# Kernel optimization log

Hardware: AMD Instinct MI355X
Metric: run time of the kernel (lower is better)

## Reference

```python
import jax, jax.numpy as jnp
import numpy as np
from jax import lax


def _rnn_layer(x_tbd, h0, Wh, bh, Wo, bo):
    """Run one RNNBlock over time. x_tbd: [T,B,D], h0: [B,H]. Returns [T,B,out]."""
    def step(h, xt):
        c = jnp.concatenate([xt, h], axis=1)        # [B, D+H]
        h_new = jnp.tanh(c @ Wh + bh)               # [B, H]
        o = jnp.tanh(c @ Wo + bo)                   # [B, out]
        return h_new, o
    _, out = lax.scan(step, h0, x_tbd)
    return out


def setup_inputs() -> dict:
    key = jax.random.key(0)
    ks = jax.random.split(key, 10)
    B, T, D, H = 64, 256, 512, 512
    s = 0.03  # small init so tanh stays non-saturated
    return {
        "x": jax.random.normal(ks[0], (B, T, D), dtype=jnp.float32),
        "encoder_output": jax.random.normal(ks[1], (B, H), dtype=jnp.float32),
        "Wh0": jax.random.normal(ks[2], (D + H, H), dtype=jnp.float32) * s,
        "bh0": jax.random.normal(ks[3], (H,), dtype=jnp.float32) * s,
        "Wo0": jax.random.normal(ks[4], (D + H, D), dtype=jnp.float32) * s,
        "bo0": jax.random.normal(ks[5], (D,), dtype=jnp.float32) * s,
        "Wh1": jax.random.normal(ks[6], (D + H, H), dtype=jnp.float32) * s,
        "bh1": jax.random.normal(ks[7], (H,), dtype=jnp.float32) * s,
        "Wo1": jax.random.normal(ks[8], (D + H, D), dtype=jnp.float32) * s,
        "bo1": jax.random.normal(ks[9], (D,), dtype=jnp.float32) * s,
    }


def reference(x, encoder_output, Wh0, bh0, Wo0, bo0, Wh1, bh1, Wo1, bo1):
    B = x.shape[0]
    H1 = Wh1.shape[1]
    x_tbd = jnp.transpose(x, (1, 0, 2))                       # [T,B,D]
    # Layer 0: initial hidden = encoder_output
    out0 = _rnn_layer(x_tbd, encoder_output, Wh0, bh0, Wo0, bo0)
    # Layer 1: hidden reset to zeros (hidden=None in torch source)
    h0 = jnp.zeros((B, H1), dtype=x.dtype)
    out1 = _rnn_layer(out0, h0, Wh1, bh1, Wo1, bo1)
    return jnp.transpose(out1, (1, 0, 2))                     # [B,T,D]
```

## Files before the change

### kernel.cpp

```cpp
#include <hip/hip_runtime.h>
#include <hip/hip_bf16.h>
#include <hip/hip_fp16.h>

typedef unsigned int u32;
typedef unsigned short u16;
typedef short s16x8 __attribute__((ext_vector_type(8)));
typedef float f32x4 __attribute__((ext_vector_type(4)));
typedef _Float16 f16x2 __attribute__((ext_vector_type(2)));

#define T_STEPS 256

__device__ __forceinline__ u16 f2bu(float f) {
  return __bfloat16_as_ushort(__float2bfloat16(f));
}
__device__ __forceinline__ float fast_tanh(float x) {
  float ax = fabsf(x);
  float e = __expf(-2.f * ax);
  float r = 1.f - 2.f * e / (1.f + e);
  return copysignf(r, x);
}
__device__ __forceinline__ __half2 bch2(u32 v) {
  return __builtin_bit_cast(__half2, v);
}
__device__ __forceinline__ void gload_lds16(const void* g, void* l) {
  __builtin_amdgcn_global_load_lds((const __attribute__((address_space(1))) u32*)g,
                                   (__attribute__((address_space(3))) u32*)l, 16, 0, 0);
}

__global__ void k_cvt_bf16(const float* __restrict__ in, u16* __restrict__ out, int n4) {
  int i = blockIdx.x * blockDim.x + threadIdx.x;
  if (i >= n4) return;
  const float4 v = ((const float4*)in)[i];
  ushort4 o;
  o.x = f2bu(v.x); o.y = f2bu(v.y); o.z = f2bu(v.z); o.w = f2bu(v.w);
  ((ushort4*)out)[i] = o;
}

__global__ void k_prep_w(const float* __restrict__ Wh, const float* __restrict__ Wo,
                         u16* __restrict__ BcatT, u16* __restrict__ WhoT,
                         u32* __restrict__ Wpack) {
  int idx = blockIdx.x * 256 + threadIdx.x;
  if (idx < 1024 * 512) {
    int n = idx >> 9, k = idx & 511;
    float v = (n < 512) ? Wh[k * 512 + n] : Wo[k * 512 + (n - 512)];
    BcatT[idx] = f2bu(v);
  } else if (idx < 1024 * 512 + 512 * 512) {
    int t = idx - 1024 * 512;
    int n = t >> 9, k = t & 511;
    WhoT[t] = f2bu(Wo[(512 + k) * 512 + n]);
  } else {
    int t = idx - (1024 * 512 + 512 * 512);
    int k2 = t >> 9, j = t & 511;
    u16 a = __half_as_ushort(__float2half(Wh[(512 + 2 * k2) * 512 + j]));
    u16 b = __half_as_ushort(__float2half(Wh[(512 + 2 * k2 + 1) * 512 + j]));
    Wpack[t] = (u32)a | ((u32)b << 16);
  }
}

template <int MODE>
__global__ __launch_bounds__(256) void k_gemm(
    const u16* __restrict__ A, const u16* __restrict__ BT, int NX,
    __half* __restrict__ outH, u16* __restrict__ outB, float* __restrict__ outF,
    const __half* __restrict__ Uo, const float* __restrict__ biasH,
    const float* __restrict__ biasO) {
  __shared__ __align__(16) u16 As[128 * 64], Bs[128 * 64];
  const int bid = blockIdx.x;
  const int bn = bid % NX, bm = bid / NX;
  const int m0 = bm * 128, n0 = bn * 128;
  const int tid = threadIdx.x, w = tid >> 6, l = tid & 63;
  const int l15 = l & 15, lk = (l >> 4) << 3;
  f32x4 acc[4][4] = {};
  for (int kt = 0; kt < 8; ++kt) {
    const int k0 = kt * 64;
#pragma unroll
    for (int i = 0; i < 4; ++i) {
      int idx = w * 4 + i;
      int ob = idx * 1024 + l * 16;
      int row = ob >> 7, cb = ob & 127;
      int scb = cb ^ ((row & 7) << 4);
      gload_lds16((const char*)A + (size_t)(m0 + row) * 1024 + k0 * 2 + scb,
                  (char*)As + idx * 1024);
      gload_lds16((const char*)BT + (size_t)(n0 + row) * 1024 + k0 * 2 + scb,
                  (char*)Bs + idx * 1024);
    }
    __syncthreads();
    const int wr = (w >> 1) * 64, wc = (w & 1) * 64;
#pragma unroll
    for (int kk = 0; kk < 2; ++kk) {
      s16x8 af[4], bfr[4];
      const int kb = (kk * 32 + lk) * 2;
#pragma unroll
      for (int i = 0; i < 4; ++i) {
        int ar = wr + i * 16 + l15;
        af[i] = *(const s16x8*)((const char*)As + ar * 128 + (kb ^ ((ar & 7) << 4)));
        int br = wc + i * 16 + l15;
        bfr[i] = *(const s16x8*)((const char*)Bs + br * 128 + (kb ^ ((br & 7) << 4)));
      }
#pragma unroll
      for (int i = 0; i < 4; ++i)
#pragma unroll
        for (int jj = 0; jj < 4; ++jj)
          acc[i][jj] = __builtin_amdgcn_mfma_f32_16x16x32_bf16(af[i], bfr[jj], acc[i][jj], 0, 0, 0);
    }
    __syncthreads();
  }
#pragma unroll
  for (int i = 0; i < 4; ++i)
#pragma unroll
    for (int jj = 0; jj < 4; ++jj)
#pragma unroll
      for (int rr = 0; rr < 4; ++rr) {
        int row = m0 + (w >> 1) * 64 + i * 16 + ((l >> 4) << 2) + rr;
        int col = n0 + (w & 1) * 64 + jj * 16 + l15;
        float v = acc[i][jj][rr];
        if (MODE == 0) {
          float bsv = (col < 512) ? biasH[col] : biasO[col - 512];
          outH[(size_t)row * 1024 + col] = __float2half(v + bsv);
        } else {
          float o = fast_tanh(v + __half2float(Uo[(size_t)row * 1024 + col]));
          if (MODE == 1) outB[(size_t)row * 512 + col] = f2bu(o);
          else           outF[(size_t)row * 512 + col] = o;
        }
      }
}

#define REG_P 192
#define LDS_GRP 16
#define SCAN_LDS_BYTES (LDS_GRP * 8192 + 2048)

__global__ __launch_bounds__(512, 2)
void k_scan(const u32* __restrict__ Wpack, const __half* __restrict__ Uh,
            const float* __restrict__ h0, u16* __restrict__ Hseq) {
  extern __shared__ __align__(16) u32 smem[];
  u32* Wl = smem;
  __half* hb = (__half*)(smem + LDS_GRP * 2048);
  const int b = blockIdx.x, j = threadIdx.x;
  u32 wreg[REG_P];
#pragma unroll
  for (int p = 0; p < REG_P; ++p) wreg[p] = Wpack[p * 512 + j];
#pragma unroll
  for (int g = 0; g < LDS_GRP; ++g)
#pragma unroll
    for (int q = 0; q < 4; ++q)
      Wl[g * 2048 + j * 4 + q] = Wpack[(REG_P + 4 * g + q) * 512 + j];
  float h = h0 ? h0[b * 512 + j] : 0.f;
  hb[j] = __float2half(h);
  __syncthreads();
  const int r0 = b * T_STEPS;
  float u_cur = __half2float(Uh[(size_t)r0 * 1024 + j]);
  for (int t = 0; t < T_STEPS; ++t) {
    const int r = r0 + t;
    const int rn = (t < T_STEPS - 1) ? r + 1 : r;
    float u_nxt = __half2float(Uh[(size_t)rn * 1024 + j]);
    Hseq[(size_t)r * 512 + j] = f2bu(h);
    const uint4* h4 = (const uint4*)(hb + (t & 1) * 512);
    __half2 a0 = __float2half2_rn(0.f), a1 = a0, a2 = a0, a3 = a0;
#pragma unroll
    for (int g = 0; g < 48; ++g) {
      uint4 hv = h4[g];
      a0 = __hfma2(bch2(wreg[4 * g + 0]), bch2(hv.x), a0);
      a1 = __hfma2(bch2(wreg[4 * g + 1]), bch2(hv.y), a1);
      a2 = __hfma2(bch2(wreg[4 * g + 2]), bch2(hv.z), a2);
      a3 = __hfma2(bch2(wreg[4 * g + 3]), bch2(hv.w), a3);
    }
#pragma unroll
    for (int g = 0; g < LDS_GRP; ++g) {
      uint4 hv = h4[48 + g];
      uint4 wv = *(const uint4*)&Wl[g * 2048 + j * 4];
      a0 = __hfma2(bch2(wv.x), bch2(hv.x), a0);
      a1 = __hfma2(bch2(wv.y), bch2(hv.y), a1);
      a2 = __hfma2(bch2(wv.z), bch2(hv.z), a2);
      a3 = __hfma2(bch2(wv.w), bch2(hv.w), a3);
    }
    float acc = u_cur;
    acc += __low2float(a0) + __high2float(a0);
    acc += __low2float(a1) + __high2float(a1);
    acc += __low2float(a2) + __high2float(a2);
    acc += __low2float(a3) + __high2float(a3);
    float hn = fast_tanh(acc);
    hb[((t + 1) & 1) * 512 + j] = __float2half(hn);
    h = hn;
    u_cur = u_nxt;
    __syncthreads();
  }
}

extern "C" void kernel_launch(void* const* d_in, const int* in_sizes, int n_in,
                              void* d_out, int out_size, void* d_ws, size_t ws_size,
                              hipStream_t stream) {
  const float* x   = (const float*)d_in[0];
  const float* enc = (const float*)d_in[1];
  const float* Wh0 = (const float*)d_in[2];
  const float* bh0 = (const float*)d_in[3];
  const float* Wo0 = (const float*)d_in[4];
  const float* bo0 = (const float*)d_in[5];
  const float* Wh1 = (const float*)d_in[6];
  const float* bh1 = (const float*)d_in[7];
  const float* Wo1 = (const float*)d_in[8];
  const float* bo1 = (const float*)d_in[9];
  char* ws = (char*)d_ws;
  u16*    Xbf   = (u16*)(ws);
  __half* U     = (__half*)(ws + 16777216);
  u16*    Hs0   = (u16*)(ws + 16777216 + 33554432);
  u16*    Out0  = (u16*)(ws + 16777216 + 33554432 + 16777216);
  u16*    Hs1   = (u16*)(ws + 16777216 + 33554432 + 2 * 16777216);
  char*   wb    = ws + 16777216 + 33554432 + 3 * 16777216;
  u16*    Bct0  = (u16*)(wb);
  u16*    WhoT0 = (u16*)(wb + 1048576);
  u32*    Wpk0  = (u32*)(wb + 1048576 + 524288);
  u16*    Bct1  = (u16*)(wb + 1048576 + 2 * 524288);
  u16*    WhoT1 = (u16*)(wb + 2 * 1048576 + 2 * 524288);
  u32*    Wpk1  = (u32*)(wb + 2 * 1048576 + 3 * 524288);

  (void)hipFuncSetAttribute((const void*)k_scan,
                            hipFuncAttributeMaxDynamicSharedMemorySize,
                            SCAN_LDS_BYTES);

  k_cvt_bf16<<<8192, 256, 0, stream>>>(x, Xbf, 8388608 / 4);
  k_prep_w<<<3584, 256, 0, stream>>>(Wh0, Wo0, Bct0, WhoT0, Wpk0);
  k_prep_w<<<3584, 256, 0, stream>>>(Wh1, Wo1, Bct1, WhoT1, Wpk1);
  k_gemm<0><<<1024, 256, 0, stream>>>(Xbf, Bct0, 8, U, nullptr, nullptr, nullptr, bh0, bo0);
  k_scan<<<64, 512, SCAN_LDS_BYTES, stream>>>(Wpk0, U, enc, Hs0);
  k_gemm<1><<<512, 256, 0, stream>>>(Hs0, WhoT0, 4, nullptr, Out0, nullptr, U + 512, nullptr, nullptr);
  k_gemm<0><<<1024, 256, 0, stream>>>(Out0, Bct1, 8, U, nullptr, nullptr, nullptr, bh1, bo1);
  k_scan<<<64, 512, SCAN_LDS_BYTES, stream>>>(Wpk1, U, nullptr, Hs1);
  k_gemm<2><<<512, 256, 0, stream>>>(Hs1, WhoT1, 4, nullptr, nullptr, (float*)d_out, U + 512, nullptr, nullptr);
}
```

Baseline: 1.027 ms.

## Fuse both RNN scans and intermediate GEMMs into one pipelined cooperative kernel

After: 1.109 ms. 8.0% more time.

```diff
diff --git a/kernel.cpp b/kernel.cpp
--- a/kernel.cpp
+++ b/kernel.cpp
@@ -25,6 +25,13 @@
 __device__ __forceinline__ void gload_lds16(const void* g, void* l) {
   __builtin_amdgcn_global_load_lds((const __attribute__((address_space(1))) u32*)g,
                                    (__attribute__((address_space(3))) u32*)l, 16, 0, 0);
+}
+__device__ __forceinline__ void wg_wait_ge(const u32* p, u32 target) {
+  if (threadIdx.x == 0) {
+    while (__hip_atomic_load(p, __ATOMIC_ACQUIRE, __HIP_MEMORY_SCOPE_AGENT) < target)
+      __builtin_amdgcn_s_sleep(16);
+  }
+  __syncthreads();
 }
 
 __global__ void k_cvt_bf16(const float* __restrict__ in, u16* __restrict__ out, int n4) {
@@ -128,13 +135,13 @@
 #define LDS_GRP 16
 #define SCAN_LDS_BYTES (LDS_GRP * 8192 + 2048)
 
-__global__ __launch_bounds__(512, 2)
-void k_scan(const u32* __restrict__ Wpack, const __half* __restrict__ Uh,
-            const float* __restrict__ h0, u16* __restrict__ Hseq) {
-  extern __shared__ __align__(16) u32 smem[];
+__device__ void scan_role(u32* smem, const u32* __restrict__ Wpack,
+                          const __half* __restrict__ Uh, const float* __restrict__ h0,
+                          u16* __restrict__ Hseq, int b,
+                          u32* rel, const u32* pollv) {
   u32* Wl = smem;
   __half* hb = (__half*)(smem + LDS_GRP * 2048);
-  const int b = blockIdx.x, j = threadIdx.x;
+  const int j = threadIdx.x;
   u32 wreg[REG_P];
 #pragma unroll
   for (int p = 0; p < REG_P; ++p) wreg[p] = Wpack[p * 512 + j];
@@ -146,13 +153,18 @@
   float h = h0 ? h0[b * 512 + j] : 0.f;
   hb[j] = __float2half(h);
   __syncthreads();
-  const int r0 = b * T_STEPS;
-  float u_cur = __half2float(Uh[(size_t)r0 * 1024 + j]);
+  const size_t r0 = (size_t)b * T_STEPS;
+  float u_cur = 0.f;
   for (int t = 0; t < T_STEPS; ++t) {
-    const int r = r0 + t;
-    const int rn = (t < T_STEPS - 1) ? r + 1 : r;
-    float u_nxt = __half2float(Uh[(size_t)rn * 1024 + j]);
-    Hseq[(size_t)r * 512 + j] = f2bu(h);
+    const size_t r = r0 + t;
+    if ((t & 31) == 0) {
+      if (pollv) wg_wait_ge(pollv + (size_t)(t >> 5) * 16, 8u);
+      if (rel && t && j == 0)
+        __hip_atomic_store(rel, (u32)t, __ATOMIC_RELEASE, __HIP_MEMORY_SCOPE_AGENT);
+      u_cur = __half2float(Uh[r * 1024 + j]);
+    }
+    Hseq[r * 512 + j] = f2bu(h);
+    float u_nxt = ((t & 31) != 31) ? __half2float(Uh[(r + 1) * 1024 + j]) : 0.f;
     const uint4* h4 = (const uint4*)(hb + (t & 1) * 512);
     __half2 a0 = __float2half2_rn(0.f), a1 = a0, a2 = a0, a3 = a0;
 #pragma unroll
@@ -182,6 +194,98 @@
     h = hn;
     u_cur = u_nxt;
     __syncthreads();
+  }
+  if (rel && j == 0)
+    __hip_atomic_store(rel, 256u, __ATOMIC_RELEASE, __HIP_MEMORY_SCOPE_AGENT);
+}
+
+__device__ void helper_role(int hid, __half* __restrict__ U,
+                            const u16* __restrict__ Hs0, u16* __restrict__ Out0,
+                            const u16* __restrict__ WhoT0, const u16* __restrict__ Bct1,
+                            const float* __restrict__ bh1, const float* __restrict__ bo1,
+                            u32* prog0, u32* o0done, u32* u1done) {
+  const int tid = threadIdx.x;
+  const int w = tid >> 6, l = tid & 63;
+  const int wr = w >> 2, wc = w & 3, l15 = l & 15, lk8 = (l >> 4) * 8;
+  for (int id = hid; id < 6144; id += 128) {
+    const int tb = id / 768, loc = id % 768;
+    if (loc < 256) {
+      const int b = loc >> 2, cq = loc & 3;
+      wg_wait_ge(prog0 + (size_t)b * 16, (u32)(32 * (tb + 1)));
+      const int r0 = b * 256 + tb * 32, c0 = cq * 128;
+      const int arow = r0 + wr * 16 + l15;
+      const int bc0 = c0 + wc * 32 + l15, bc1 = bc0 + 16;
+      f32x4 a0 = {}, a1 = {};
+#pragma unroll
+      for (int k0 = 0; k0 < 512; k0 += 32) {
+        s16x8 av = *(const s16x8*)&Hs0[(size_t)arow * 512 + k0 + lk8];
+        s16x8 b0 = *(const s16x8*)&WhoT0[(size_t)bc0 * 512 + k0 + lk8];
+        s16x8 b1 = *(const s16x8*)&WhoT0[(size_t)bc1 * 512 + k0 + lk8];
+        a0 = __builtin_amdgcn_mfma_f32_16x16x32_bf16(av, b0, a0, 0, 0, 0);
+        a1 = __builtin_amdgcn_mfma_f32_16x16x32_bf16(av, b1, a1, 0, 0, 0);
+      }
+#pragma unroll
+      for (int rr = 0; rr < 4; ++rr) {
+        int row = r0 + wr * 16 + (l >> 4) * 4 + rr;
+        int cA = c0 + wc * 32 + l15, cB = cA + 16;
+        float vA = fast_tanh(a0[rr] + __half2float(U[(size_t)row * 1024 + 512 + cA]));
+        float vB = fast_tanh(a1[rr] + __half2float(U[(size_t)row * 1024 + 512 + cB]));
+        Out0[(size_t)row * 512 + cA] = f2bu(vA);
+        Out0[(size_t)row * 512 + cB] = f2bu(vB);
+      }
+      __syncthreads();
+      if (tid == 0)
+        __hip_atomic_fetch_add(o0done + ((size_t)b * 8 + tb) * 16, 1u,
+                               __ATOMIC_RELEASE, __HIP_MEMORY_SCOPE_AGENT);
+    } else {
+      const int loc2 = loc - 256;
+      const int b = loc2 >> 3, cc = loc2 & 7;
+      wg_wait_ge(o0done + ((size_t)b * 8 + tb) * 16, 4u);
+      const int r0 = b * 256 + tb * 32, c0 = cc * 128;
+      const int arow = r0 + wr * 16 + l15;
+      const int bc0 = c0 + wc * 32 + l15, bc1 = bc0 + 16;
+      f32x4 a0 = {}, a1 = {};
+#pragma unroll
+      for (int k0 = 0; k0 < 512; k0 += 32) {
+        s16x8 av = *(const s16x8*)&Out0[(size_t)arow * 512 + k0 + lk8];
+        s16x8 b0 = *(const s16x8*)&Bct1[(size_t)bc0 * 512 + k0 + lk8];
+        s16x8 b1 = *(const s16x8*)&Bct1[(size_t)bc1 * 512 + k0 + lk8];
+        a0 = __builtin_amdgcn_mfma_f32_16x16x32_bf16(av, b0, a0, 0, 0, 0);
+        a1 = __builtin_amdgcn_mfma_f32_16x16x32_bf16(av, b1, a1, 0, 0, 0);
+      }
+#pragma unroll
+      for (int rr = 0; rr < 4; ++rr) {
+        int row = r0 + wr * 16 + (l >> 4) * 4 + rr;
+        int cA = c0 + wc * 32 + l15, cB = cA + 16;
+        float bA = (cA < 512) ? bh1[cA] : bo1[cA - 512];
+        float bB = (cB < 512) ? bh1[cB] : bo1[cB - 512];
+        U[(size_t)row * 1024 + cA] = __float2half(a0[rr] + bA);
+        U[(size_t)row * 1024 + cB] = __float2half(a1[rr] + bB);
+      }
+      __syncthreads();
+      if (tid == 0)
+        __hip_atomic_fetch_add(u1done + ((size_t)b * 8 + tb) * 16, 1u,
+                               __ATOMIC_RELEASE, __HIP_MEMORY_SCOPE_AGENT);
+    }
+  }
+}
+
+__global__ __launch_bounds__(512, 2) void k_mega(
+    const u32* __restrict__ Wpk0, const u32* __restrict__ Wpk1,
+    __half* __restrict__ U, const float* __restrict__ enc,
+    u16* __restrict__ Hs0, u16* __restrict__ Hs1, u16* __restrict__ Out0,
+    const u16* __restrict__ WhoT0, const u16* __restrict__ Bct1,
+    const float* __restrict__ bh1, const float* __restrict__ bo1,
+    u32* prog0, u32* o0done, u32* u1done) {
+  extern __shared__ __align__(16) u32 smem[];
+  const int wg = blockIdx.x;
+  if (wg < 64) {
+    scan_role(smem, Wpk0, U, enc, Hs0, wg, prog0 + (size_t)wg * 16, nullptr);
+  } else if (wg < 128) {
+    const int b = wg - 64;
+    scan_role(smem, Wpk1, U, nullptr, Hs1, b, nullptr, u1done + (size_t)b * 8 * 16);
+  } else {
+    helper_role(wg - 128, U, Hs0, Out0, WhoT0, Bct1, bh1, bo1, prog0, o0done, u1done);
   }
 }
 
@@ -199,30 +303,43 @@
   const float* Wo1 = (const float*)d_in[8];
   const float* bo1 = (const float*)d_in[9];
   char* ws = (char*)d_ws;
-  u16*    Xbf   = (u16*)(ws);
-  __half* U     = (__half*)(ws + 16777216);
-  u16*    Hs0   = (u16*)(ws + 16777216 + 33554432);
-  u16*    Out0  = (u16*)(ws + 16777216 + 33554432 + 16777216);
-  u16*    Hs1   = (u16*)(ws + 16777216 + 33554432 + 2 * 16777216);
-  char*   wb    = ws + 16777216 + 33554432 + 3 * 16777216;
+  __half* U    = (__half*)(ws);
+  u16*    Hs0  = (u16*)(ws + 33554432);
+  u16*    Hs1  = (u16*)(ws + 33554432 + 16777216);
+  u16*    XO   = (u16*)(ws + 33554432 + 2 * 16777216);
+  char*   wb   = ws + 33554432 + 3 * 16777216;
   u16*    Bct0  = (u16*)(wb);
   u16*    WhoT0 = (u16*)(wb + 1048576);
   u32*    Wpk0  = (u32*)(wb + 1048576 + 524288);
   u16*    Bct1  = (u16*)(wb + 1048576 + 2 * 524288);
   u16*    WhoT1 = (u16*)(wb + 2 * 1048576 + 2 * 524288);
   u32*    Wpk1  = (u32*)(wb + 2 * 1048576 + 3 * 524288);
-
-  (void)hipFuncSetAttribute((const void*)k_scan,
+  u32*    cnt   = (u32*)(wb + 2 * 1048576 + 4 * 524288);
+  u32*    prog0  = cnt;
+  u32*    o0done = cnt + 1024;
+  u32*    u1done = cnt + 1024 + 8192;
+
+  (void)hipFuncSetAttribute((const void*)k_mega,
                             hipFuncAttributeMaxDynamicSharedMemorySize,
                             SCAN_LDS_BYTES);
 
-  k_cvt_bf16<<<8192, 256, 0, stream>>>(x, Xbf, 8388608 / 4);
+  hipMemsetAsync(cnt, 0, (1024 + 2 * 8192) * 4, stream);
+  k_cvt_bf16<<<8192, 256, 0, stream>>>(x, XO, 8388608 / 4);
   k_prep_w<<<3584, 256, 0, stream>>>(Wh0, Wo0, Bct0, WhoT0, Wpk0);
   k_prep_w<<<3584, 256, 0, stream>>>(Wh1, Wo1, Bct1, WhoT1, Wpk1);
-  k_gemm<0><<<1024, 256, 0, stream>>>(Xbf, Bct0, 8, U, nullptr, nullptr, nullptr, bh0, bo0);
-  k_scan<<<64, 512, SCAN_LDS_BYTES, stream>>>(Wpk0, U, enc, Hs0);
-  k_gemm<1><<<512, 256, 0, stream>>>(Hs0, WhoT0, 4, nullptr, Out0, nullptr, U + 512, nullptr, nullptr);
-  k_gemm<0><<<1024, 256, 0, stream>>>(Out0, Bct1, 8, U, nullptr, nullptr, nullptr, bh1, bo1);
-  k_scan<<<64, 512, SCAN_LDS_BYTES, stream>>>(Wpk1, U, nullptr, Hs1);
-  k_gemm<2><<<512, 256, 0, stream>>>(Hs1, WhoT1, 4, nullptr, nullptr, (float*)d_out, U + 512, nullptr, nullptr);
-}
+  k_gemm<0><<<1024, 256, 0, stream>>>(XO, Bct0, 8, U, nullptr, nullptr, nullptr, bh0, bo0);
+
+  {
+    const u32* a0 = Wpk0; const u32* a1 = Wpk1; __half* a2 = U;
+    const float* a3 = enc; u16* a4 = Hs0; u16* a5 = Hs1; u16* a6 = XO;
+    const u16* a7 = WhoT0; const u16* a8 = Bct1;
+    const float* a9 = bh1; const float* a10 = bo1;
+    u32* a11 = prog0; u32* a12 = o0done; u32* a13 = u1done;
+    void* args[] = {&a0, &a1, &a2, &a3, &a4, &a5, &a6, &a7, &a8, &a9, &a10, &a11, &a12, &a13};
+    hipLaunchCooperativeKernel((const void*)k_mega, dim3(256), dim3(512), args,
+                               SCAN_LDS_BYTES, stream);
+  }
+
+  k_gemm<2><<<512, 256, 0, stream>>>(Hs1, WhoT1, 4, nullptr, nullptr, (float*)d_out,
+                                     U + 512, nullptr, nullptr);
+}
```

## Split recurrent scan K-dimension across 8 lanes with DPP reduction and streamed weights

Applied to the files above, without the earlier changes.

Result: slower. 1.620 ms (+57.8%).

```diff
diff --git a/kernel.cpp b/kernel.cpp
--- a/kernel.cpp
+++ b/kernel.cpp
@@ -6,7 +6,6 @@
 typedef unsigned short u16;
 typedef short s16x8 __attribute__((ext_vector_type(8)));
 typedef float f32x4 __attribute__((ext_vector_type(4)));
-typedef _Float16 f16x2 __attribute__((ext_vector_type(2)));
 
 #define T_STEPS 256
 
@@ -25,6 +24,11 @@
 __device__ __forceinline__ void gload_lds16(const void* g, void* l) {
   __builtin_amdgcn_global_load_lds((const __attribute__((address_space(1))) u32*)g,
                                    (__attribute__((address_space(3))) u32*)l, 16, 0, 0);
+}
+template <int CTRL>
+__device__ __forceinline__ float dppadd(float x) {
+  int r = __builtin_amdgcn_update_dpp(0, __builtin_bit_cast(int, x), CTRL, 0xf, 0xf, true);
+  return x + __builtin_bit_cast(float, r);
 }
 
 __global__ void k_cvt_bf16(const float* __restrict__ in, u16* __restrict__ out, int n4) {
@@ -49,11 +53,25 @@
     int n = t >> 9, k = t & 511;
     WhoT[t] = f2bu(Wo[(512 + k) * 512 + n]);
   } else {
-    int t = idx - (1024 * 512 + 512 * 512);
-    int k2 = t >> 9, j = t & 511;
-    u16 a = __half_as_ushort(__float2half(Wh[(512 + 2 * k2) * 512 + j]));
-    u16 b = __half_as_ushort(__float2half(Wh[(512 + 2 * k2 + 1) * 512 + j]));
-    Wpack[t] = (u32)a | ((u32)b << 16);
+    int w2 = idx - (1024 * 512 + 512 * 512);
+    int p, i, j;
+    if (w2 < 65536) {
+      p = w2 >> 13; i = (w2 >> 9) & 15; j = w2 & 511;
+    } else if (w2 < 81920) {
+      int t = w2 - 65536;
+      p = t >> 11; j = (t >> 2) & 511; i = 16 + (t & 3);
+    } else {
+      int t = w2 - 81920;
+      int row = t >> 11;
+      p = row / 3; int g = row - 3 * p;
+      j = (t >> 2) & 511; i = 20 + g * 4 + (t & 3);
+    }
+    int ks = j & 7, c = j >> 3;
+    int C = p * 64 + c;
+    int k = ks * 64 + 2 * i;
+    u16 a = __half_as_ushort(__float2half(Wh[(512 + k) * 512 + C]));
+    u16 b = __half_as_ushort(__float2half(Wh[(512 + k + 1) * 512 + C]));
+    Wpack[w2] = (u32)a | ((u32)b << 16);
   }
 }
 
@@ -124,64 +142,108 @@
       }
 }
 
-#define REG_P 192
-#define LDS_GRP 16
-#define SCAN_LDS_BYTES (LDS_GRP * 8192 + 2048)
-
-__global__ __launch_bounds__(512, 2)
-void k_scan(const u32* __restrict__ Wpack, const __half* __restrict__ Uh,
-            const float* __restrict__ h0, u16* __restrict__ Hseq) {
+#define HB_SLICE 144
+#define HB_PAR (8 * HB_SLICE)
+#define SCAN3_LDS_BYTES (65536 + 2 * HB_PAR)
+
+__global__ __launch_bounds__(512) __attribute__((amdgpu_waves_per_eu(2, 2)))
+void k_scan3(const u32* __restrict__ Wpk, const __half* __restrict__ Uh,
+             const float* __restrict__ h0, u16* __restrict__ Hseq) {
   extern __shared__ __align__(16) u32 smem[];
   u32* Wl = smem;
-  __half* hb = (__half*)(smem + LDS_GRP * 2048);
+  char* hb = (char*)(smem + 16384);
   const int b = blockIdx.x, j = threadIdx.x;
-  u32 wreg[REG_P];
-#pragma unroll
-  for (int p = 0; p < REG_P; ++p) wreg[p] = Wpack[p * 512 + j];
-#pragma unroll
-  for (int g = 0; g < LDS_GRP; ++g)
-#pragma unroll
-    for (int q = 0; q < 4; ++q)
-      Wl[g * 2048 + j * 4 + q] = Wpack[(REG_P + 4 * g + q) * 512 + j];
-  float h = h0 ? h0[b * 512 + j] : 0.f;
-  hb[j] = __float2half(h);
+  const int ks = j & 7, c = j >> 3;
+  const size_t r0 = (size_t)b * T_STEPS;
+
+  u32 wreg[128];
+#pragma unroll
+  for (int p8 = 0; p8 < 128; ++p8) wreg[p8] = Wpk[p8 * 512 + j];
+  {
+    const u32* src = Wpk + 65536;
+#pragma unroll
+    for (int p = 0; p < 8; ++p)
+      gload_lds16(src + (p * 512 + j) * 4, (char*)Wl + (p * 512 + (j & ~63)) * 16);
+  }
+  {
+    float hv = h0 ? h0[b * 512 + j] : 0.f;
+    *(__half*)(hb + (j >> 6) * HB_SLICE + (j & 63) * 2) = __float2half(hv);
+    Hseq[r0 * 512 + j] = f2bu(hv);
+  }
+  const u32* Wst = Wpk + 81920;
+  u32 sbufA[12], sbufB[12];
+#pragma unroll
+  for (int g = 0; g < 3; ++g) {
+    uint4 v = *(const uint4*)(Wst + ((0 * 3 + g) * 512 + j) * 4);
+    sbufA[g * 4 + 0] = v.x; sbufA[g * 4 + 1] = v.y;
+    sbufA[g * 4 + 2] = v.z; sbufA[g * 4 + 3] = v.w;
+  }
+  float u_pre[8];
+#pragma unroll
+  for (int p = 0; p < 8; ++p) u_pre[p] = __half2float(Uh[r0 * 1024 + p * 64 + c]);
   __syncthreads();
-  const int r0 = b * T_STEPS;
-  float u_cur = __half2float(Uh[(size_t)r0 * 1024 + j]);
+
+  int par = 0;
   for (int t = 0; t < T_STEPS; ++t) {
-    const int r = r0 + t;
-    const int rn = (t < T_STEPS - 1) ? r + 1 : r;
-    float u_nxt = __half2float(Uh[(size_t)rn * 1024 + j]);
-    Hseq[(size_t)r * 512 + j] = f2bu(h);
-    const uint4* h4 = (const uint4*)(hb + (t & 1) * 512);
-    __half2 a0 = __float2half2_rn(0.f), a1 = a0, a2 = a0, a3 = a0;
-#pragma unroll
-    for (int g = 0; g < 48; ++g) {
-      uint4 hv = h4[g];
-      a0 = __hfma2(bch2(wreg[4 * g + 0]), bch2(hv.x), a0);
-      a1 = __hfma2(bch2(wreg[4 * g + 1]), bch2(hv.y), a1);
-      a2 = __hfma2(bch2(wreg[4 * g + 2]), bch2(hv.z), a2);
-      a3 = __hfma2(bch2(wreg[4 * g + 3]), bch2(hv.w), a3);
-    }
-#pragma unroll
-    for (int g = 0; g < LDS_GRP; ++g) {
-      uint4 hv = h4[48 + g];
-      uint4 wv = *(const uint4*)&Wl[g * 2048 + j * 4];
-      a0 = __hfma2(bch2(wv.x), bch2(hv.x), a0);
-      a1 = __hfma2(bch2(wv.y), bch2(hv.y), a1);
-      a2 = __hfma2(bch2(wv.z), bch2(hv.z), a2);
-      a3 = __hfma2(bch2(wv.w), bch2(hv.w), a3);
-    }
-    float acc = u_cur;
-    acc += __low2float(a0) + __high2float(a0);
-    acc += __low2float(a1) + __high2float(a1);
-    acc += __low2float(a2) + __high2float(a2);
-    acc += __low2float(a3) + __high2float(a3);
-    float hn = fast_tanh(acc);
-    hb[((t + 1) & 1) * 512 + j] = __float2half(hn);
-    h = hn;
-    u_cur = u_nxt;
+    u32 hsv[32];
+    {
+      const char* hbp = hb + par * HB_PAR + ks * HB_SLICE;
+#pragma unroll
+      for (int i = 0; i < 8; ++i) {
+        uint4 v = *(const uint4*)(hbp + i * 16);
+        hsv[i * 4 + 0] = v.x; hsv[i * 4 + 1] = v.y;
+        hsv[i * 4 + 2] = v.z; hsv[i * 4 + 3] = v.w;
+      }
+    }
+    float u_cur[8];
+#pragma unroll
+    for (int p = 0; p < 8; ++p) u_cur[p] = u_pre[p];
+    if (t + 1 < T_STEPS) {
+#pragma unroll
+      for (int p = 0; p < 8; ++p)
+        u_pre[p] = __half2float(Uh[(r0 + t + 1) * 1024 + p * 64 + c]);
+    }
+#pragma unroll
+    for (int p = 0; p < 8; ++p) {
+      u32* scur = (p & 1) ? sbufB : sbufA;
+      u32* snxt = (p & 1) ? sbufA : sbufB;
+#pragma unroll
+      for (int g = 0; g < 3; ++g) {
+        uint4 v = *(const uint4*)(Wst + ((((p + 1) & 7) * 3 + g) * 512 + j) * 4);
+        snxt[g * 4 + 0] = v.x; snxt[g * 4 + 1] = v.y;
+        snxt[g * 4 + 2] = v.z; snxt[g * 4 + 3] = v.w;
+      }
+      uint4 wlv = *(const uint4*)((const char*)Wl + (p * 512 + j) * 16);
+      u32 wlw[4] = {wlv.x, wlv.y, wlv.z, wlv.w};
+      __half2 a0 = __float2half2_rn(0.f), a1 = a0;
+#pragma unroll
+      for (int i = 0; i < 16; ++i) {
+        __half2& a = (i & 1) ? a1 : a0;
+        a = __hfma2(bch2(wreg[p * 16 + i]), bch2(hsv[i]), a);
+      }
+#pragma unroll
+      for (int i = 0; i < 4; ++i) {
+        __half2& a = (i & 1) ? a1 : a0;
+        a = __hfma2(bch2(wlw[i]), bch2(hsv[16 + i]), a);
+      }
+#pragma unroll
+      for (int i = 0; i < 12; ++i) {
+        __half2& a = (i & 1) ? a1 : a0;
+        a = __hfma2(bch2(scur[i]), bch2(hsv[20 + i]), a);
+      }
+      float sm = __low2float(a0) + __high2float(a0) +
+                 __low2float(a1) + __high2float(a1);
+      sm = dppadd<0xB1>(sm);
+      sm = dppadd<0x4E>(sm);
+      sm = dppadd<0x141>(sm);
+      float f = fast_tanh(sm + u_cur[p]);
+      if (ks == 0)
+        *(__half*)(hb + (par ^ 1) * HB_PAR + p * HB_SLICE + c * 2) = __float2half(f);
+      if (ks == 1 && t + 1 < T_STEPS)
+        Hseq[(r0 + t + 1) * 512 + p * 64 + c] = f2bu(f);
+    }
     __syncthreads();
+    par ^= 1;
   }
 }
 
@@ -212,17 +274,17 @@
   u16*    WhoT1 = (u16*)(wb + 2 * 1048576 + 2 * 524288);
   u32*    Wpk1  = (u32*)(wb + 2 * 1048576 + 3 * 524288);
 
-  (void)hipFuncSetAttribute((const void*)k_scan,
+  (void)hipFuncSetAttribute((const void*)k_scan3,
                             hipFuncAttributeMaxDynamicSharedMemorySize,
-                            SCAN_LDS_BYTES);
+                            SCAN3_LDS_BYTES);
 
   k_cvt_bf16<<<8192, 256, 0, stream>>>(x, Xbf, 8388608 / 4);
   k_prep_w<<<3584, 256, 0, stream>>>(Wh0, Wo0, Bct0, WhoT0, Wpk0);
   k_prep_w<<<3584, 256, 0, stream>>>(Wh1, Wo1, Bct1, WhoT1, Wpk1);
   k_gemm<0><<<1024, 256, 0, stream>>>(Xbf, Bct0, 8, U, nullptr, nullptr, nullptr, bh0, bo0);
-  k_scan<<<64, 512, SCAN_LDS_BYTES, stream>>>(Wpk0, U, enc, Hs0);
+  k_scan3<<<64, 512, SCAN3_LDS_BYTES, stream>>>(Wpk0, U, enc, Hs0);
   k_gemm<1><<<512, 256, 0, stream>>>(Hs0, WhoT0, 4, nullptr, Out0, nullptr, U + 512, nullptr, nullptr);
   k_gemm<0><<<1024, 256, 0, stream>>>(Out0, Bct1, 8, U, nullptr, nullptr, nullptr, bh1, bo1);
-  k_scan<<<64, 512, SCAN_LDS_BYTES, stream>>>(Wpk1, U, nullptr, Hs1);
+  k_scan3<<<64, 512, SCAN3_LDS_BYTES, stream>>>(Wpk1, U, nullptr, Hs1);
   k_gemm<2><<<512, 256, 0, stream>>>(Hs1, WhoT1, 4, nullptr, nullptr, (float*)d_out, U + 512, nullptr, nullptr);
 }
```

## Split recurrent dot product across 4 lanes with DPP reduction to cut LDS h reads

Applied to the files above, without the earlier changes.

After: 1.217 ms. +18.5%, slower.

```diff
diff --git a/kernel.cpp b/kernel.cpp
--- a/kernel.cpp
+++ b/kernel.cpp
@@ -6,7 +6,6 @@
 typedef unsigned short u16;
 typedef short s16x8 __attribute__((ext_vector_type(8)));
 typedef float f32x4 __attribute__((ext_vector_type(4)));
-typedef _Float16 f16x2 __attribute__((ext_vector_type(2)));
 
 #define T_STEPS 256
 
@@ -25,6 +24,11 @@
 __device__ __forceinline__ void gload_lds16(const void* g, void* l) {
   __builtin_amdgcn_global_load_lds((const __attribute__((address_space(1))) u32*)g,
                                    (__attribute__((address_space(3))) u32*)l, 16, 0, 0);
+}
+template <int CTRL>
+__device__ __forceinline__ float dppadd(float x) {
+  int r = __builtin_amdgcn_update_dpp(0, __builtin_bit_cast(int, x), CTRL, 0xf, 0xf, true);
+  return x + __builtin_bit_cast(float, r);
 }
 
 __global__ void k_cvt_bf16(const float* __restrict__ in, u16* __restrict__ out, int n4) {
@@ -49,11 +53,26 @@
     int n = t >> 9, k = t & 511;
     WhoT[t] = f2bu(Wo[(512 + k) * 512 + n]);
   } else {
-    int t = idx - (1024 * 512 + 512 * 512);
-    int k2 = t >> 9, j = t & 511;
-    u16 a = __half_as_ushort(__float2half(Wh[(512 + 2 * k2) * 512 + j]));
-    u16 b = __half_as_ushort(__float2half(Wh[(512 + 2 * k2 + 1) * 512 + j]));
-    Wpack[t] = (u32)a | ((u32)b << 16);
+    int w2 = idx - (1024 * 512 + 512 * 512);
+    int i, j, col;
+    if (w2 < 98304) {
+      int p = w2 >> 9; j = w2 & 511;
+      int g = p >> 4, r = p & 15;
+      col = r >> 2; int q = r & 3;
+      i = 4 * g + q;
+    } else {
+      int t = w2 - 98304;
+      int q = t & 3; j = (t >> 2) & 511;
+      int grp = t >> 11;
+      col = grp >> 2; int g2 = grp & 3;
+      i = 48 + g2 * 4 + q;
+    }
+    int ks = j & 3, c0 = j >> 2;
+    int C = col * 128 + c0;
+    int k = ks * 128 + 2 * i;
+    u16 a = __half_as_ushort(__float2half(Wh[(512 + k) * 512 + C]));
+    u16 b = __half_as_ushort(__float2half(Wh[(512 + k + 1) * 512 + C]));
+    Wpack[w2] = (u32)a | ((u32)b << 16);
   }
 }
 
@@ -124,64 +143,114 @@
       }
 }
 
-#define REG_P 192
-#define LDS_GRP 16
-#define SCAN_LDS_BYTES (LDS_GRP * 8192 + 2048)
+#define SCAN4_LDS_BYTES (131072 + 2048)
 
 __global__ __launch_bounds__(512, 2)
-void k_scan(const u32* __restrict__ Wpack, const __half* __restrict__ Uh,
-            const float* __restrict__ h0, u16* __restrict__ Hseq) {
+void k_scan4(const u32* __restrict__ Wpk, const __half* __restrict__ Uh,
+             const float* __restrict__ h0, u16* __restrict__ Hseq) {
   extern __shared__ __align__(16) u32 smem[];
-  u32* Wl = smem;
-  __half* hb = (__half*)(smem + LDS_GRP * 2048);
+  uint4* Wl4 = (uint4*)smem;
+  char* hb = (char*)smem + 131072;
   const int b = blockIdx.x, j = threadIdx.x;
-  u32 wreg[REG_P];
-#pragma unroll
-  for (int p = 0; p < REG_P; ++p) wreg[p] = Wpack[p * 512 + j];
-#pragma unroll
-  for (int g = 0; g < LDS_GRP; ++g)
-#pragma unroll
-    for (int q = 0; q < 4; ++q)
-      Wl[g * 2048 + j * 4 + q] = Wpack[(REG_P + 4 * g + q) * 512 + j];
-  float h = h0 ? h0[b * 512 + j] : 0.f;
-  hb[j] = __float2half(h);
+  const int ks = j & 3, c0 = j >> 2;
+  const size_t r0 = (size_t)b * T_STEPS;
+  u32 wreg[192];
+#pragma unroll
+  for (int p = 0; p < 192; ++p) wreg[p] = Wpk[p * 512 + j];
+#pragma unroll
+  for (int g = 0; g < 16; ++g)
+    Wl4[g * 512 + j] = *(const uint4*)(Wpk + 98304 + ((size_t)g * 512 + j) * 4);
+  {
+    float hv = h0 ? h0[b * 512 + j] : 0.f;
+    *(__half*)(hb + j * 2) = __float2half(hv);
+    Hseq[r0 * 512 + j] = f2bu(hv);
+  }
+  float u0 = __half2float(Uh[r0 * 1024 + c0]);
+  float u1 = __half2float(Uh[r0 * 1024 + 128 + c0]);
+  float u2 = __half2float(Uh[r0 * 1024 + 256 + c0]);
+  float u3 = __half2float(Uh[r0 * 1024 + 384 + c0]);
   __syncthreads();
-  const int r0 = b * T_STEPS;
-  float u_cur = __half2float(Uh[(size_t)r0 * 1024 + j]);
+  int par = 0;
   for (int t = 0; t < T_STEPS; ++t) {
-    const int r = r0 + t;
-    const int rn = (t < T_STEPS - 1) ? r + 1 : r;
-    float u_nxt = __half2float(Uh[(size_t)rn * 1024 + j]);
-    Hseq[(size_t)r * 512 + j] = f2bu(h);
-    const uint4* h4 = (const uint4*)(hb + (t & 1) * 512);
-    __half2 a0 = __float2half2_rn(0.f), a1 = a0, a2 = a0, a3 = a0;
-#pragma unroll
-    for (int g = 0; g < 48; ++g) {
+    float un0 = 0.f, un1 = 0.f, un2 = 0.f, un3 = 0.f;
+    if (t + 1 < T_STEPS) {
+      const __half* up = Uh + (r0 + t + 1) * 1024;
+      un0 = __half2float(up[c0]);       un1 = __half2float(up[128 + c0]);
+      un2 = __half2float(up[256 + c0]); un3 = __half2float(up[384 + c0]);
+    }
+    const uint4* h4 = (const uint4*)(hb + par * 1024 + ks * 256);
+    const __half2 zero = __float2half2_rn(0.f);
+    __half2 aA0 = zero, aA1 = zero, aB0 = zero, aB1 = zero;
+    __half2 aC0 = zero, aC1 = zero, aD0 = zero, aD1 = zero;
+#pragma unroll
+    for (int g = 0; g < 12; ++g) {
       uint4 hv = h4[g];
-      a0 = __hfma2(bch2(wreg[4 * g + 0]), bch2(hv.x), a0);
-      a1 = __hfma2(bch2(wreg[4 * g + 1]), bch2(hv.y), a1);
-      a2 = __hfma2(bch2(wreg[4 * g + 2]), bch2(hv.z), a2);
-      a3 = __hfma2(bch2(wreg[4 * g + 3]), bch2(hv.w), a3);
-    }
-#pragma unroll
-    for (int g = 0; g < LDS_GRP; ++g) {
-      uint4 hv = h4[48 + g];
-      uint4 wv = *(const uint4*)&Wl[g * 2048 + j * 4];
-      a0 = __hfma2(bch2(wv.x), bch2(hv.x), a0);
-      a1 = __hfma2(bch2(wv.y), bch2(hv.y), a1);
-      a2 = __hfma2(bch2(wv.z), bch2(hv.z), a2);
-      a3 = __hfma2(bch2(wv.w), bch2(hv.w), a3);
-    }
-    float acc = u_cur;
-    acc += __low2float(a0) + __high2float(a0);
-    acc += __low2float(a1) + __high2float(a1);
-    acc += __low2float(a2) + __high2float(a2);
-    acc += __low2float(a3) + __high2float(a3);
-    float hn = fast_tanh(acc);
-    hb[((t + 1) & 1) * 512 + j] = __float2half(hn);
-    h = hn;
-    u_cur = u_nxt;
+      aA0 = __hfma2(bch2(wreg[g * 16 + 0]), bch2(hv.x), aA0);
+      aA1 = __hfma2(bch2(wreg[g * 16 + 1]), bch2(hv.y), aA1);
+      aA0 = __hfma2(bch2(wreg[g * 16 + 2]), bch2(hv.z), aA0);
+      aA1 = __hfma2(bch2(wreg[g * 16 + 3]), bch2(hv.w), aA1);
+      aB0 = __hfma2(bch2(wreg[g * 16 + 4]), bch2(hv.x), aB0);
+      aB1 = __hfma2(bch2(wreg[g * 16 + 5]), bch2(hv.y), aB1);
+      aB0 = __hfma2(bch2(wreg[g * 16 + 6]), bch2(hv.z), aB0);
+      aB1 = __hfma2(bch2(wreg[g * 16 + 7]), bch2(hv.w), aB1);
+      aC0 = __hfma2(bch2(wreg[g * 16 + 8]), bch2(hv.x), aC0);
+      aC1 = __hfma2(bch2(wreg[g * 16 + 9]), bch2(hv.y), aC1);
+      aC0 = __hfma2(bch2(wreg[g * 16 + 10]), bch2(hv.z), aC0);
+      aC1 = __hfma2(bch2(wreg[g * 16 + 11]), bch2(hv.w), aC1);
+      aD0 = __hfma2(bch2(wreg[g * 16 + 12]), bch2(hv.x), aD0);
+      aD1 = __hfma2(bch2(wreg[g * 16 + 13]), bch2(hv.y), aD1);
+      aD0 = __hfma2(bch2(wreg[g * 16 + 14]), bch2(hv.z), aD0);
+      aD1 = __hfma2(bch2(wreg[g * 16 + 15]), bch2(hv.w), aD1);
+    }
+#pragma unroll
+    for (int g2 = 0; g2 < 4; ++g2) {
+      uint4 hv = h4[12 + g2];
+      uint4 wA = Wl4[(0 + g2) * 512 + j];
+      uint4 wB = Wl4[(4 + g2) * 512 + j];
+      uint4 wC = Wl4[(8 + g2) * 512 + j];
+      uint4 wD = Wl4[(12 + g2) * 512 + j];
+      aA0 = __hfma2(bch2(wA.x), bch2(hv.x), aA0);
+      aA1 = __hfma2(bch2(wA.y), bch2(hv.y), aA1);
+      aA0 = __hfma2(bch2(wA.z), bch2(hv.z), aA0);
+      aA1 = __hfma2(bch2(wA.w), bch2(hv.w), aA1);
+      aB0 = __hfma2(bch2(wB.x), bch2(hv.x), aB0);
+      aB1 = __hfma2(bch2(wB.y), bch2(hv.y), aB1);
+      aB0 = __hfma2(bch2(wB.z), bch2(hv.z), aB0);
+      aB1 = __hfma2(bch2(wB.w), bch2(hv.w), aB1);
+      aC0 = __hfma2(bch2(wC.x), bch2(hv.x), aC0);
+      aC1 = __hfma2(bch2(wC.y), bch2(hv.y), aC1);
+      aC0 = __hfma2(bch2(wC.z), bch2(hv.z), aC0);
+      aC1 = __hfma2(bch2(wC.w), bch2(hv.w), aC1);
+      aD0 = __hfma2(bch2(wD.x), bch2(hv.x), aD0);
+      aD1 = __hfma2(bch2(wD.y), bch2(hv.y), aD1);
+      aD0 = __hfma2(bch2(wD.z), bch2(hv.z), aD0);
+      aD1 = __hfma2(bch2(wD.w), bch2(hv.w), aD1);
+    }
+    float s0 = __low2float(aA0) + __high2float(aA0) + __low2float(aA1) + __high2float(aA1);
+    float s1 = __low2float(aB0) + __high2float(aB0) + __low2float(aB1) + __high2float(aB1);
+    float s2 = __low2float(aC0) + __high2float(aC0) + __low2float(aC1) + __high2float(aC1);
+    float s3 = __low2float(aD0) + __high2float(aD0) + __low2float(aD1) + __high2float(aD1);
+    s0 = dppadd<0xB1>(s0); s0 = dppadd<0x4E>(s0);
+    s1 = dppadd<0xB1>(s1); s1 = dppadd<0x4E>(s1);
+    s2 = dppadd<0xB1>(s2); s2 = dppadd<0x4E>(s2);
+    s3 = dppadd<0xB1>(s3); s3 = dppadd<0x4E>(s3);
+    float f0 = fast_tanh(s0 + u0), f1 = fast_tanh(s1 + u1);
+    float f2 = fast_tanh(s2 + u2), f3 = fast_tanh(s3 + u3);
+    char* hbn = hb + (par ^ 1) * 1024;
+    if (ks == 0) {
+      *(__half*)(hbn + c0 * 2) = __float2half(f0);
+      *(__half*)(hbn + (128 + c0) * 2) = __float2half(f1);
+      *(__half*)(hbn + (256 + c0) * 2) = __float2half(f2);
+      *(__half*)(hbn + (384 + c0) * 2) = __float2half(f3);
+    }
+    if (ks == 1 && t + 1 < T_STEPS) {
+      u16* hp = Hseq + (r0 + t + 1) * 512;
+      hp[c0] = f2bu(f0); hp[128 + c0] = f2bu(f1);
+      hp[256 + c0] = f2bu(f2); hp[384 + c0] = f2bu(f3);
+    }
+    u0 = un0; u1 = un1; u2 = un2; u3 = un3;
     __syncthreads();
+    par ^= 1;
   }
 }
 
@@ -212,17 +281,17 @@
   u16*    WhoT1 = (u16*)(wb + 2 * 1048576 + 2 * 524288);
   u32*    Wpk1  = (u32*)(wb + 2 * 1048576 + 3 * 524288);
 
-  (void)hipFuncSetAttribute((const void*)k_scan,
+  (void)hipFuncSetAttribute((const void*)k_scan4,
                             hipFuncAttributeMaxDynamicSharedMemorySize,
-                            SCAN_LDS_BYTES);
+                            SCAN4_LDS_BYTES);
 
   k_cvt_bf16<<<8192, 256, 0, stream>>>(x, Xbf, 8388608 / 4);
   k_prep_w<<<3584, 256, 0, stream>>>(Wh0, Wo0, Bct0, WhoT0, Wpk0);
   k_prep_w<<<3584, 256, 0, stream>>>(Wh1, Wo1, Bct1, WhoT1, Wpk1);
   k_gemm<0><<<1024, 256, 0, stream>>>(Xbf, Bct0, 8, U, nullptr, nullptr, nullptr, bh0, bo0);
-  k_scan<<<64, 512, SCAN_LDS_BYTES, stream>>>(Wpk0, U, enc, Hs0);
+  k_scan4<<<64, 512, SCAN4_LDS_BYTES, stream>>>(Wpk0, U, enc, Hs0);
   k_gemm<1><<<512, 256, 0, stream>>>(Hs0, WhoT0, 4, nullptr, Out0, nullptr, U + 512, nullptr, nullptr);
   k_gemm<0><<<1024, 256, 0, stream>>>(Out0, Bct1, 8, U, nullptr, nullptr, nullptr, bh1, bo1);
-  k_scan<<<64, 512, SCAN_LDS_BYTES, stream>>>(Wpk1, U, nullptr, Hs1);
+  k_scan4<<<64, 512, SCAN4_LDS_BYTES, stream>>>(Wpk1, U, nullptr, Hs1);
   k_gemm<2><<<512, 256, 0, stream>>>(Hs1, WhoT1, 4, nullptr, nullptr, (float*)d_out, U + 512, nullptr, nullptr);
 }
```
